# Optimization experiments

Hardware: AMD Instinct MI355X
Metric: run time of the kernel (lower is better)

Reference implementation:

```python
import jax, jax.numpy as jnp
import numpy as np

A = -0.75  # torch bicubic coefficient

def _cubic_weights(t):
    # t in [0,1): weights for taps at offsets -1,0,1,2 (torch aten formulation)
    x = t + 1.0
    w0 = ((A * x - 5.0 * A) * x + 8.0 * A) * x - 4.0 * A
    w1 = ((A + 2.0) * t - (A + 3.0)) * t * t + 1.0
    s = 1.0 - t
    w2 = ((A + 2.0) * s - (A + 3.0)) * s * s + 1.0
    w3 = 1.0 - w0 - w1 - w2
    return jnp.stack([w0, w1, w2, w3], axis=-1)

def _grid_sample_bicubic(feat, gx, gy):
    # feat [B,C,H,W]; gx,gy [B,Q] normalized coords; align_corners=False, zero padding
    B, C, H, W = feat.shape
    ix = ((gx + 1.0) * W - 1.0) * 0.5
    iy = ((gy + 1.0) * H - 1.0) * 0.5
    ix0 = jnp.floor(ix)
    iy0 = jnp.floor(iy)
    wx = _cubic_weights(ix - ix0)  # [B,Q,4]
    wy = _cubic_weights(iy - iy0)
    ix0 = ix0.astype(jnp.int32)
    iy0 = iy0.astype(jnp.int32)
    feat_flat = feat.reshape(B, C, H * W)
    out = jnp.zeros((B, C, gx.shape[1]), feat.dtype)
    for i in range(4):  # fixed 4x4 tap stencil
        yi = iy0 - 1 + i
        yok = (yi >= 0) & (yi < H)
        yc = jnp.clip(yi, 0, H - 1)
        for j in range(4):
            xj = ix0 - 1 + j
            ok = yok & (xj >= 0) & (xj < W)
            xc = jnp.clip(xj, 0, W - 1)
            v = jnp.take_along_axis(feat_flat, (yc * W + xc)[:, None, :], axis=2)  # [B,C,Q]
            w = wy[..., i] * wx[..., j] * ok
            out = out + v * w[:, None, :]
    return out

def _make_coord(H, W):
    # LIIF make_coord: cell-centered coords in (-1,1), dim order (y, x)
    y = -1.0 + (2.0 * jnp.arange(H, dtype=jnp.float32) + 1.0) / H
    x = -1.0 + (2.0 * jnp.arange(W, dtype=jnp.float32) + 1.0) / W
    yy, xx = jnp.meshgrid(y, x, indexing='ij')
    return jnp.stack([yy, xx], axis=-1)  # [H,W,2]

def _mlp(h, params):
    n = len(params)
    for i, (w, b) in enumerate(params):
        h = h @ w + b
        if i < n - 1:
            h = jax.nn.relu(h)
    return h

def _forward(x, mlp_p, rout_p, off_p, scale):
    B, C, H, W = x.shape
    Ho, Wo = H * scale, W * scale
    Q = Ho * Wo
    coord = jnp.broadcast_to(_make_coord(Ho, Wo).reshape(1, Q, 2), (B, Q, 2))
    cell = jnp.ones((B, Q, 2), x.dtype)
    # faithful to original: cell[:, 0] *= 2/H ; cell[:, 1] *= 2/W indexes the QUERY dim
    cell = cell.at[:, 0].multiply(2.0 / Ho).at[:, 1].multiply(2.0 / Wo)
    cc = jnp.clip(coord, -1.0 + 1e-6, 1.0 - 1e-6)
    gy, gx = cc[..., 0], cc[..., 1]  # flip(-1): grid x = width coord
    q_feat = _grid_sample_bicubic(x, gx, gy).transpose(0, 2, 1)  # [B,Q,C]
    fc = jnp.broadcast_to(_make_coord(H, W).transpose(2, 0, 1)[None], (B, 2, H, W))
    q_coord = _grid_sample_bicubic(fc, gx, gy).transpose(0, 2, 1)  # [B,Q,2]
    hw = jnp.array([H, W], x.dtype)
    rel_coord = (coord - q_coord) * hw
    rel_cell = cell * hw
    inp = jnp.concatenate([q_feat, rel_coord, rel_cell], axis=-1)  # [B,Q,C+4]
    pred = _mlp(inp, mlp_p)          # [B,Q,C]
    routing = _mlp(pred, rout_p)     # [B,Q,C]
    off = _mlp(pred, off_p)          # [B,Q,2]
    gx2 = gx + off[..., 0]
    gy2 = gy + off[..., 1]
    q_feat1 = _grid_sample_bicubic(x, gx2, gy2).transpose(0, 2, 1)
    out = q_feat1 * (1.0 + routing)  # q_feat1 + q_feat1*routing
    return out.transpose(0, 2, 1).reshape(B, C, Ho, Wo)

def setup_inputs():
    key = jax.random.key(0)
    ks = jax.random.split(key, 16)
    B, C, H, W = 4, 32, 128, 128
    def lin(k, i, o):
        return 0.02 * jax.random.normal(k, (i, o), jnp.float32)
    def bias(k, o):
        return 0.02 * jax.random.normal(k, (o,), jnp.float32)
    return {
        "x": jax.random.normal(ks[0], (B, C, H, W), jnp.float32),
        "mlp_w0": lin(ks[1], 36, 256), "mlp_b0": bias(ks[2], 256),
        "mlp_w1": lin(ks[3], 256, 256), "mlp_b1": bias(ks[4], 256),
        "mlp_w2": lin(ks[5], 256, 32), "mlp_b2": bias(ks[6], 32),
        "rout_w0": lin(ks[7], 32, 256), "rout_b0": bias(ks[8], 256),
        "rout_w1": lin(ks[9], 256, 32), "rout_b1": bias(ks[10], 32),
        "off_w0": lin(ks[11], 32, 256), "off_b0": bias(ks[12], 256),
        "off_w1": lin(ks[13], 256, 2), "off_b1": bias(ks[14], 2),
        "scale": 2,
    }

def reference(x, mlp_w0, mlp_b0, mlp_w1, mlp_b1, mlp_w2, mlp_b2,
              rout_w0, rout_b0, rout_w1, rout_b1,
              off_w0, off_b0, off_w1, off_b1, scale):
    mlp_p = [(mlp_w0, mlp_b0), (mlp_w1, mlp_b1), (mlp_w2, mlp_b2)]
    rout_p = [(rout_w0, rout_b0), (rout_w1, rout_b1)]
    off_p = [(off_w0, off_b0), (off_w1, off_b1)]
    return _forward(x, mlp_p, rout_p, off_p, int(scale))
```

## Files before the change

### kernel.cpp

```cpp
#include <hip/hip_runtime.h>
#include <hip/hip_bf16.h>
#include <stdint.h>

#define BB 4
#define CCH 32
#define HH 128
#define WW 128
#define SCALE 2
#define HO 256
#define WO 256
#define QQ (HO*WO)
#define HWH (HH*WW)
#define MT 128
#define KPAD 264
#define PSTR 40

#define WOFF_L0 0
#define WOFF_L1 16384
#define WOFF_L2 81920
#define WOFF_R0 90112
#define WOFF_R1 98304
#define WOFF_O0 106496
#define WOFF_O1 114688
#define WTOT    118784

typedef unsigned short u16;
typedef __attribute__((ext_vector_type(8))) __bf16 bf16x8;
typedef __attribute__((ext_vector_type(4))) float f32x4;

__device__ __forceinline__ f32x4 MFMA(bf16x8 a, bf16x8 b, f32x4 c) {
  return __builtin_amdgcn_mfma_f32_16x16x32_bf16(a, b, c, 0, 0, 0);
}

__device__ __forceinline__ u16 f2bf(float f) {
  union { float f; unsigned int u; } v; v.f = f;
  unsigned int u = v.u;
  u += 0x7fffu + ((u >> 16) & 1u);
  return (u16)(u >> 16);
}

__device__ __forceinline__ uint32_t pkbf(float a, float b) {
  union { __hip_bfloat162 h; uint32_t u; } cv;
  cv.h = __float22bfloat162_rn(make_float2(a, b));
  return cv.u;
}

__device__ __forceinline__ float bf2f(u16 u) {
  union { unsigned int u; float f; } v; v.u = ((unsigned int)u) << 16;
  return v.f;
}

__global__ void prep_weights(const float* __restrict__ w0, const float* __restrict__ w1,
                             const float* __restrict__ w2, const float* __restrict__ r0,
                             const float* __restrict__ r1, const float* __restrict__ o0,
                             const float* __restrict__ o1, u16* __restrict__ wt)
{
  int idx = blockIdx.x * 256 + threadIdx.x;
  if (idx >= WTOT) return;
  const float* src; int K, Nsrc, KP, base;
  if (idx < WOFF_L1)      { src = w0; K = 36;  Nsrc = 256; KP = 64;  base = WOFF_L0; }
  else if (idx < WOFF_L2) { src = w1; K = 256; Nsrc = 256; KP = 256; base = WOFF_L1; }
  else if (idx < WOFF_R0) { src = w2; K = 256; Nsrc = 32;  KP = 256; base = WOFF_L2; }
  else if (idx < WOFF_R1) { src = r0; K = 32;  Nsrc = 256; KP = 32;  base = WOFF_R0; }
  else if (idx < WOFF_O0) { src = r1; K = 256; Nsrc = 32;  KP = 256; base = WOFF_R1; }
  else if (idx < WOFF_O1) { src = o0; K = 32;  Nsrc = 256; KP = 32;  base = WOFF_O0; }
  else                    { src = o1; K = 256; Nsrc = 2;   KP = 256; base = WOFF_O1; }
  int local = idx - base;
  int n = local / KP, k = local % KP;
  float v = (k < K && n < Nsrc) ? src[k * Nsrc + n] : 0.f;
  wt[idx] = f2bf(v);
}

__device__ __forceinline__ void cubw(float t, float w[4]) {
  const float A = -0.75f;
  float x = t + 1.f;
  w[0] = ((A * x - 5.f * A) * x + 8.f * A) * x - 4.f * A;
  w[1] = ((A + 2.f) * t - (A + 3.f)) * t * t + 1.f;
  float s = 1.f - t;
  w[2] = ((A + 2.f) * s - (A + 3.f)) * s * s + 1.f;
  w[3] = 1.f - w[0] - w[1] - w[2];
}

__device__ __forceinline__ void bicubic8(const float* __restrict__ bptr, float gx, float gy,
                                         float feat[8], float& qcy, float& qcx)
{
  float ix = ((gx + 1.f) * (float)WW - 1.f) * 0.5f;
  float iy = ((gy + 1.f) * (float)HH - 1.f) * 0.5f;
  float fx0 = floorf(ix), fy0 = floorf(iy);
  float tx = ix - fx0, ty = iy - fy0;
  float wx[4], wy[4];
  cubw(tx, wx); cubw(ty, wy);
  int ix0 = (int)fx0, iy0 = (int)fy0;
  #pragma unroll
  for (int c = 0; c < 8; c++) feat[c] = 0.f;
  qcy = 0.f; qcx = 0.f;
  #pragma unroll
  for (int i = 0; i < 4; i++) {
    int yi = iy0 - 1 + i;
    bool yok = (yi >= 0) && (yi < HH);
    int yc = min(max(yi, 0), HH - 1);
    float yv = -1.f + (2.f * yc + 1.f) * (1.f / HH);
    #pragma unroll
    for (int j = 0; j < 4; j++) {
      int xj = ix0 - 1 + j;
      bool ok = yok && (xj >= 0) && (xj < WW);
      if (!ok) continue;
      int xc = min(max(xj, 0), WW - 1);
      float wv = wy[i] * wx[j];
      const float* p = bptr + yc * WW + xc;
      #pragma unroll
      for (int c = 0; c < 8; c++) feat[c] = fmaf(wv, p[c * HWH], feat[c]);
      qcy = fmaf(wv, yv, qcy);
      qcx = fmaf(wv, (-1.f + (2.f * xc + 1.f) * (1.f / WW)), qcx);
    }
  }
}


template<int KP, int LSTR, bool RELU, bool INPLACE>
__device__ __forceinline__ void layer_n256(const u16* lin, u16* lout,
                                           const u16* __restrict__ W,
                                           const float* __restrict__ bias, int w, int lane)
{
  int lm = lane & 15, quad = lane >> 4;
  int nbase = w * 64;
  f32x4 acc[8][4];
  #pragma unroll
  for (int nt = 0; nt < 4; nt++) {
    float bv = bias[nbase + nt * 16 + lm];
    f32x4 b4 = {bv, bv, bv, bv};
    #pragma unroll
    for (int mt = 0; mt < 8; mt++) acc[mt][nt] = b4;
  }
  #pragma unroll
  for (int kk = 0; kk < KP / 32; kk++) {
    bf16x8 bf[4];
    #pragma unroll
    for (int nt = 0; nt < 4; nt++)
      bf[nt] = *(const bf16x8*)(W + (nbase + nt * 16 + lm) * KP + kk * 32 + quad * 8);
    #pragma unroll
    for (int mt = 0; mt < 8; mt++) {
      bf16x8 af = *(const bf16x8*)(lin + (mt * 16 + lm) * LSTR + kk * 32 + quad * 8);
      #pragma unroll
      for (int nt = 0; nt < 4; nt++)
        acc[mt][nt] = MFMA(af, bf[nt], acc[mt][nt]);
    }
  }
  if (INPLACE) __syncthreads();
  #pragma unroll
  for (int mt = 0; mt < 8; mt++)
    #pragma unroll
    for (int nt = 0; nt < 4; nt++) {
      int col = nbase + nt * 16 + lm;
      u16* base = lout + (mt * 16 + quad * 4) * KPAD + col;
      #pragma unroll
      for (int r = 0; r < 4; r += 2) {
        float v0 = acc[mt][nt][r], v1 = acc[mt][nt][r + 1];
        if (RELU) { v0 = fmaxf(v0, 0.f); v1 = fmaxf(v1, 0.f); }
        uint32_t p = pkbf(v0, v1);
        base[r * KPAD]       = (u16)p;
        base[(r + 1) * KPAD] = (u16)(p >> 16);
      }
    }
}

__device__ __forceinline__ void layer_n32(const u16* lin, u16* lout,
                                          const u16* __restrict__ W,
                                          const float* __restrict__ bias, int w, int lane)
{
  int lm = lane & 15, quad = lane >> 4;
  int nt = w & 1, mtb = (w >> 1) * 4;
  float bv = bias[nt * 16 + lm];
  f32x4 acc[4];
  #pragma unroll
  for (int mi = 0; mi < 4; mi++) acc[mi] = (f32x4){bv, bv, bv, bv};
  #pragma unroll
  for (int kk = 0; kk < 8; kk++) {
    bf16x8 bf = *(const bf16x8*)(W + (nt * 16 + lm) * 256 + kk * 32 + quad * 8);
    #pragma unroll
    for (int mi = 0; mi < 4; mi++) {
      bf16x8 af = *(const bf16x8*)(lin + ((mtb + mi) * 16 + lm) * KPAD + kk * 32 + quad * 8);
      acc[mi] = MFMA(af, bf, acc[mi]);
    }
  }
  #pragma unroll
  for (int mi = 0; mi < 4; mi++) {
    int row0 = (mtb + mi) * 16 + quad * 4, col = nt * 16 + lm;
    #pragma unroll
    for (int r = 0; r < 4; r += 2) {
      float v0 = acc[mi][r], v1 = acc[mi][r + 1];
      uint32_t p = pkbf(v0, v1);
      lout[(row0 + r) * PSTR + col]     = (u16)p;
      lout[(row0 + r + 1) * PSTR + col] = (u16)(p >> 16);
    }
  }
}

__device__ __forceinline__ void layer_off(const u16* lin, float* offb,
                                          const u16* __restrict__ W,
                                          const float* __restrict__ bias, int w, int lane)
{
  int lm = lane & 15, quad = lane >> 4;
  int mtb = w * 2;
  float bv = (lm < 2) ? bias[lm] : 0.f;
  f32x4 acc[2];
  acc[0] = (f32x4){bv, bv, bv, bv};
  acc[1] = acc[0];
  #pragma unroll
  for (int kk = 0; kk < 8; kk++) {
    bf16x8 bf = *(const bf16x8*)(W + lm * 256 + kk * 32 + quad * 8);
    #pragma unroll
    for (int mi = 0; mi < 2; mi++) {
      bf16x8 af = *(const bf16x8*)(lin + ((mtb + mi) * 16 + lm) * KPAD + kk * 32 + quad * 8);
      acc[mi] = MFMA(af, bf, acc[mi]);
    }
  }
  if (lm < 2) {
    #pragma unroll
    for (int mi = 0; mi < 2; mi++)
      #pragma unroll
      for (int r = 0; r < 4; r++)
        offb[((mtb + mi) * 16 + quad * 4 + r) * 2 + lm] = acc[mi][r];
  }
}

__launch_bounds__(256, 2)
__global__ void liif_fused(const float* __restrict__ x, const u16* __restrict__ wt,
                           const float* __restrict__ b0, const float* __restrict__ b1,
                           const float* __restrict__ b2, const float* __restrict__ rb0,
                           const float* __restrict__ rb1, const float* __restrict__ ob0,
                           const float* __restrict__ ob1, float* __restrict__ out)
{
  __shared__ __align__(16) u16 act[MT * KPAD];
  __shared__ __align__(16) u16 predb[MT * PSTR];
  __shared__ float offb[MT * 2];
  __shared__ float gxy[MT * 2];

  int t = threadIdx.x;
  int g = t >> 6;
  int lane = t & 63;
  int b = (blockIdx.x * MT) >> 16;
  const float* bptr = x + (b * CCH + g * 8) * HWH;

  #pragma unroll
  for (int s = 0; s < 2; s++) {
    int ql = lane + s * 64;
    int qi = (blockIdx.x * MT + ql) & (QQ - 1);
    int oy = qi >> 8, ox = qi & (WO - 1);
    float coordy = -1.f + (2.f * oy + 1.f) * (1.f / HO);
    float coordx = -1.f + (2.f * ox + 1.f) * (1.f / WO);
    float gy = fminf(fmaxf(coordy, -1.f + 1e-6f), 1.f - 1e-6f);
    float gx = fminf(fmaxf(coordx, -1.f + 1e-6f), 1.f - 1e-6f);
    float feat[8], qcy, qcx;
    bicubic8(bptr, gx, gy, feat, qcy, qcx);
    union { uint32_t u[4]; bf16x8 v; } pk;
    #pragma unroll
    for (int c = 0; c < 4; c++) pk.u[c] = pkbf(feat[2 * c], feat[2 * c + 1]);
    *(bf16x8*)&act[ql * KPAD + g * 8] = pk.v;
    if (g == 0) {
      gxy[ql * 2 + 0] = gx;
      gxy[ql * 2 + 1] = gy;
      float rcy = (coordy - qcy) * (float)HH;
      float rcx = (coordx - qcx) * (float)WW;
      float m = (qi == 0) ? (2.f / HO) : (qi == 1) ? (2.f / WO) : 1.f;
      act[ql * KPAD + 32] = f2bf(rcy);
      act[ql * KPAD + 33] = f2bf(rcx);
      act[ql * KPAD + 34] = f2bf(m * (float)HH);
      act[ql * KPAD + 35] = f2bf(m * (float)WW);
    } else if (g == 1) {
      uint64_t* z = (uint64_t*)&act[ql * KPAD + 36];
      #pragma unroll
      for (int k = 0; k < 7; k++) z[k] = 0ull;
    }
  }
  __syncthreads();

  layer_n256<64, KPAD, true, true>(act, act, wt + WOFF_L0, b0, g, lane);
  __syncthreads();
  layer_n256<256, KPAD, true, true>(act, act, wt + WOFF_L1, b1, g, lane);
  __syncthreads();
  layer_n32(act, predb, wt + WOFF_L2, b2, g, lane);
  __syncthreads();
  layer_n256<32, PSTR, true, false>(predb, act, wt + WOFF_O0, ob0, g, lane);
  __syncthreads();
  layer_off(act, offb, wt + WOFF_O1, ob1, g, lane);
  __syncthreads();
  layer_n256<32, PSTR, true, false>(predb, act, wt + WOFF_R0, rb0, g, lane);
  __syncthreads();
  layer_n32(act, predb, wt + WOFF_R1, rb1, g, lane);
  __syncthreads();

  #pragma unroll
  for (int s = 0; s < 2; s++) {
    int ql = lane + s * 64;
    int qi = (blockIdx.x * MT + ql) & (QQ - 1);
    int oy = qi >> 8, ox = qi & (WO - 1);
    float gx2 = gxy[ql * 2 + 0] + offb[ql * 2 + 0];
    float gy2 = gxy[ql * 2 + 1] + offb[ql * 2 + 1];
    float feat[8], d0, d1;
    bicubic8(bptr, gx2, gy2, feat, d0, d1);
    const u16* rp = &predb[ql * PSTR + g * 8];
    float* op = out + (b * CCH + g * 8) * (HO * WO) + oy * WO + ox;
    #pragma unroll
    for (int c = 0; c < 8; c++)
      op[c * (HO * WO)] = feat[c] * (1.f + bf2f(rp[c]));
  }
}

extern "C" void kernel_launch(void* const* d_in, const int* in_sizes, int n_in,
                              void* d_out, int out_size, void* d_ws, size_t ws_size,
                              hipStream_t stream)
{
  const float* x   = (const float*)d_in[0];
  const float* w0  = (const float*)d_in[1];
  const float* b0  = (const float*)d_in[2];
  const float* w1  = (const float*)d_in[3];
  const float* b1  = (const float*)d_in[4];
  const float* w2  = (const float*)d_in[5];
  const float* b2  = (const float*)d_in[6];
  const float* r0  = (const float*)d_in[7];
  const float* rb0 = (const float*)d_in[8];
  const float* r1  = (const float*)d_in[9];
  const float* rb1 = (const float*)d_in[10];
  const float* o0  = (const float*)d_in[11];
  const float* ob0 = (const float*)d_in[12];
  const float* o1  = (const float*)d_in[13];
  const float* ob1 = (const float*)d_in[14];
  u16* wt = (u16*)d_ws;
  float* out = (float*)d_out;

  prep_weights<<<(WTOT + 255) / 256, 256, 0, stream>>>(w0, w1, w2, r0, r1, o0, o1, wt);
  liif_fused<<<(BB * QQ) / MT, 256, 0, stream>>>(x, wt, b0, b1, b2, rb0, rb1, ob0, ob1, out);
}
```

Baseline: 252.3 us.

## Vectorize bicubic row loads and precompute lattice weights for first sample

Replaces the per-tap scalar bicubic gather with a clamped 4-wide window per row, loaded as float4, with the x weights shifted to match the clamped base and out-of-range rows zeroed. The coordinate outputs are factorised into separable sums. For the first sampling pass the query lies on the exact 2x lattice, so constant cubic weights picked by parity replace the floor and polynomial evaluation. The aim is fewer load instructions and less ALU work per sample. Unaligned float4 loads and the separable qc formula may shift rounding slightly.

New measurement: 221.2 us. -12.3%, faster.

```diff
diff --git a/kernel.cpp b/kernel.cpp
--- a/kernel.cpp
+++ b/kernel.cpp
@@ -81,39 +81,86 @@
   w[3] = 1.f - w[0] - w[1] - w[2];
 }
 
-__device__ __forceinline__ void bicubic8(const float* __restrict__ bptr, float gx, float gy,
-                                         float feat[8], float& qcy, float& qcx)
+__device__ __forceinline__ void bicubic8_rows(const float* __restrict__ bptr,
+                                              int ix0, int iy0,
+                                              const float wx[4], const float wy[4],
+                                              float feat[8], float& qcy, float& qcx)
+{
+  int bx = min(max(ix0 - 1, 0), WW - 4);
+  int d = bx - (ix0 - 1);
+  float wl[4];
+  #pragma unroll
+  for (int i = 0; i < 4; i++) {
+    int j = i + d;
+    float w = 0.f;
+    w = (j == 0) ? wx[0] : w;
+    w = (j == 1) ? wx[1] : w;
+    w = (j == 2) ? wx[2] : w;
+    w = (j == 3) ? wx[3] : w;
+    wl[i] = w;
+  }
+  float wyl[4]; int yrow[4];
+  #pragma unroll
+  for (int i = 0; i < 4; i++) {
+    int y = iy0 - 1 + i;
+    wyl[i] = (y >= 0 && y < HH) ? wy[i] : 0.f;
+    yrow[i] = min(max(y, 0), HH - 1);
+  }
+  float w16[4][4];
+  #pragma unroll
+  for (int i = 0; i < 4; i++)
+    #pragma unroll
+    for (int j = 0; j < 4; j++) w16[i][j] = wyl[i] * wl[j];
+
+  #pragma unroll
+  for (int c = 0; c < 8; c++) feat[c] = 0.f;
+  float ydot = 0.f, wysum = 0.f;
+  #pragma unroll
+  for (int i = 0; i < 4; i++) {
+    const float* rp = bptr + yrow[i] * WW + bx;
+    #pragma unroll
+    for (int c = 0; c < 8; c++) {
+      float4 p;
+      __builtin_memcpy(&p, rp + c * HWH, 16);
+      feat[c] = fmaf(w16[i][0], p.x, feat[c]);
+      feat[c] = fmaf(w16[i][1], p.y, feat[c]);
+      feat[c] = fmaf(w16[i][2], p.z, feat[c]);
+      feat[c] = fmaf(w16[i][3], p.w, feat[c]);
+    }
+    float yv = -1.f + (2.f * yrow[i] + 1.f) * (1.f / HH);
+    ydot = fmaf(wyl[i], yv, ydot);
+    wysum += wyl[i];
+  }
+  float wlsum = (wl[0] + wl[1]) + (wl[2] + wl[3]);
+  float xb = -1.f + (2.f * bx + 1.f) * (1.f / WW);
+  float xdot = wl[0] * xb;
+  xdot = fmaf(wl[1], xb + 2.f / WW, xdot);
+  xdot = fmaf(wl[2], xb + 4.f / WW, xdot);
+  xdot = fmaf(wl[3], xb + 6.f / WW, xdot);
+  qcy = wlsum * ydot;
+  qcx = wysum * xdot;
+}
+
+__device__ __forceinline__ void bicubic8_any(const float* __restrict__ bptr, float gx, float gy,
+                                             float feat[8], float& qcy, float& qcx)
 {
   float ix = ((gx + 1.f) * (float)WW - 1.f) * 0.5f;
   float iy = ((gy + 1.f) * (float)HH - 1.f) * 0.5f;
   float fx0 = floorf(ix), fy0 = floorf(iy);
-  float tx = ix - fx0, ty = iy - fy0;
   float wx[4], wy[4];
-  cubw(tx, wx); cubw(ty, wy);
-  int ix0 = (int)fx0, iy0 = (int)fy0;
-  #pragma unroll
-  for (int c = 0; c < 8; c++) feat[c] = 0.f;
-  qcy = 0.f; qcx = 0.f;
-  #pragma unroll
-  for (int i = 0; i < 4; i++) {
-    int yi = iy0 - 1 + i;
-    bool yok = (yi >= 0) && (yi < HH);
-    int yc = min(max(yi, 0), HH - 1);
-    float yv = -1.f + (2.f * yc + 1.f) * (1.f / HH);
-    #pragma unroll
-    for (int j = 0; j < 4; j++) {
-      int xj = ix0 - 1 + j;
-      bool ok = yok && (xj >= 0) && (xj < WW);
-      if (!ok) continue;
-      int xc = min(max(xj, 0), WW - 1);
-      float wv = wy[i] * wx[j];
-      const float* p = bptr + yc * WW + xc;
-      #pragma unroll
-      for (int c = 0; c < 8; c++) feat[c] = fmaf(wv, p[c * HWH], feat[c]);
-      qcy = fmaf(wv, yv, qcy);
-      qcx = fmaf(wv, (-1.f + (2.f * xc + 1.f) * (1.f / WW)), qcx);
-    }
-  }
+  cubw(ix - fx0, wx);
+  cubw(iy - fy0, wy);
+  bicubic8_rows(bptr, (int)fx0, (int)fy0, wx, wy, feat, qcy, qcx);
+}
+
+__device__ __forceinline__ void latt_w(int o, float w[4], int& i0) {
+  const float W0 = -0.10546875f, W1 = 0.87890625f, W2 = 0.26171875f, W3 = -0.03515625f;
+  bool odd = (o & 1);
+  w[0] = odd ? W0 : W3;
+  w[1] = odd ? W1 : W2;
+  w[2] = odd ? W2 : W1;
+  w[3] = odd ? W3 : W0;
+  i0 = (o - 1) >> 1;
 }
 
 
@@ -251,8 +298,11 @@
     float coordx = -1.f + (2.f * ox + 1.f) * (1.f / WO);
     float gy = fminf(fmaxf(coordy, -1.f + 1e-6f), 1.f - 1e-6f);
     float gx = fminf(fmaxf(coordx, -1.f + 1e-6f), 1.f - 1e-6f);
+    float wx[4], wy[4]; int ix0, iy0;
+    latt_w(ox, wx, ix0);
+    latt_w(oy, wy, iy0);
     float feat[8], qcy, qcx;
-    bicubic8(bptr, gx, gy, feat, qcy, qcx);
+    bicubic8_rows(bptr, ix0, iy0, wx, wy, feat, qcy, qcx);
     union { uint32_t u[4]; bf16x8 v; } pk;
     #pragma unroll
     for (int c = 0; c < 4; c++) pk.u[c] = pkbf(feat[2 * c], feat[2 * c + 1]);
@@ -298,7 +348,7 @@
     float gx2 = gxy[ql * 2 + 0] + offb[ql * 2 + 0];
     float gy2 = gxy[ql * 2 + 1] + offb[ql * 2 + 1];
     float feat[8], d0, d1;
-    bicubic8(bptr, gx2, gy2, feat, d0, d1);
+    bicubic8_any(bptr, gx2, gy2, feat, d0, d1);
     const u16* rp = &predb[ql * PSTR + g * 8];
     float* op = out + (b * CCH + g * 8) * (HO * WO) + oy * WO + ox;
     #pragma unroll
```
